# Performance work log

Measured on AMD Instinct MI355X. Metric: run time of the kernel, lower is better.

## Reference

```python
import jax, jax.numpy as jnp
import numpy as np

H = 256

def setup_inputs() -> dict:
    key = jax.random.key(0)
    ks = jax.random.split(key, 9)
    s = 1.0 / np.sqrt(H)
    x = jax.random.normal(ks[0], (8, 2048, H), dtype=jnp.float32)
    Wq = jax.random.uniform(ks[1], (H, H), jnp.float32, -s, s)
    bq = jax.random.uniform(ks[2], (H,), jnp.float32, -s, s)
    Wk = jax.random.uniform(ks[3], (H, H), jnp.float32, -s, s)
    bk = jax.random.uniform(ks[4], (H,), jnp.float32, -s, s)
    Wv = jax.random.uniform(ks[5], (H, H), jnp.float32, -s, s)
    bv = jax.random.uniform(ks[6], (H,), jnp.float32, -s, s)
    Ww = jax.random.uniform(ks[7], (H, 1), jnp.float32, -s, s)
    bw = jax.random.uniform(ks[8], (1,), jnp.float32, -s, s)
    return {"x": x, "Wq": Wq, "bq": bq, "Wk": Wk, "bk": bk,
            "Wv": Wv, "bv": bv, "Ww": Ww, "bw": bw}

def reference(x, Wq, bq, Wk, bk, Wv, bv, Ww, bw):
    # x: (B, N, H) — cross-asset attention over N assets
    q = x @ Wq + bq
    k = x @ Wk + bk
    v = x @ Wv + bv
    scale = 1.0 / jnp.sqrt(jnp.asarray(q.shape[-1], q.dtype))
    beta = jnp.einsum('bnd,bmd->bnm', q, k) * scale  # (B, N, N)
    beta = jax.nn.softmax(beta, axis=-1)
    # original: sum(value[:,None] * beta[...,None], dim=2) == beta @ v
    out = jnp.einsum('bnm,bmd->bnd', beta, v)
    final_scores = (out @ Ww + bw)[..., 0]  # (B, N)
    return final_scores
```

## Files before the change

### kernel.cpp

```cpp
#include <hip/hip_runtime.h>

#define H 256
#define NB 2048
#define BATCH 8
#define NSPLIT 4
#define KSPAN (NB / NSPLIT)

typedef unsigned short u16;
using bf16x8 = __attribute__((ext_vector_type(8))) __bf16;
using f32x4  = __attribute__((ext_vector_type(4))) float;

__device__ __forceinline__ u16 f2bf(float f) {
    union { float f; unsigned u; } v; v.f = f;
    unsigned r = v.u + 0x7fffu + ((v.u >> 16) & 1u);
    return (u16)(r >> 16);
}

__global__ __launch_bounds__(256) void weights_kernel(
        const float* __restrict__ Wq, const float* __restrict__ Wk,
        const float* __restrict__ Wv, const float* __restrict__ Ww,
        u16* __restrict__ wqt, u16* __restrict__ wkt, float* __restrict__ wvw) {
    int n = blockIdx.x, k = threadIdx.x;
    wqt[n * H + k] = f2bf(Wq[k * H + n]);
    wkt[n * H + k] = f2bf(Wk[k * H + n]);
    float p = Wv[n * H + k] * Ww[k];
    for (int o = 32; o; o >>= 1) p += __shfl_xor(p, o);
    __shared__ float red[4];
    int w = threadIdx.x >> 6, lane = threadIdx.x & 63;
    if (lane == 0) red[w] = p;
    __syncthreads();
    if (threadIdx.x == 0) wvw[n] = red[0] + red[1] + red[2] + red[3];
}

__global__ __launch_bounds__(256) void cvtu_kernel(
        const float* __restrict__ x, const float* __restrict__ wvw,
        const float* __restrict__ bv, const float* __restrict__ Ww,
        u16* __restrict__ xbf, float* __restrict__ uu) {
    int lane = threadIdx.x & 63;
    int row  = blockIdx.x * 4 + (threadIdx.x >> 6);
    float4 xv = *(const float4*)(x + row * H + lane * 4);
    ushort4 o;
    o.x = f2bf(xv.x); o.y = f2bf(xv.y); o.z = f2bf(xv.z); o.w = f2bf(xv.w);
    *(ushort4*)(xbf + row * H + lane * 4) = o;
    float4 wv = *(const float4*)(wvw + lane * 4);
    float s = xv.x * wv.x + xv.y * wv.y + xv.z * wv.z + xv.w * wv.w;
    float4 bvv = *(const float4*)(bv + lane * 4);
    float4 www = *(const float4*)(Ww + lane * 4);
    float c = bvv.x * www.x + bvv.y * www.y + bvv.z * www.z + bvv.w * www.w;
    for (int o2 = 32; o2; o2 >>= 1) { s += __shfl_xor(s, o2); c += __shfl_xor(c, o2); }
    if (lane == 0) uu[row] = s + c;
}

__global__ __launch_bounds__(256) void proj_kernel(
        const u16* __restrict__ xbf, const u16* __restrict__ wqt, const u16* __restrict__ wkt,
        const float* __restrict__ bq, const float* __restrict__ bk,
        u16* __restrict__ qbf, u16* __restrict__ kbf) {
    __shared__ u16 bt[64 * 264];
    const u16* wt      = blockIdx.z ? wkt : wqt;
    const float* bias  = blockIdx.z ? bk : bq;
    u16* outp          = blockIdx.z ? kbf : qbf;
    const float sc     = blockIdx.z ? 1.0f : 0.0625f;

    int tid = threadIdx.x;
    int mb = blockIdx.x * 64, nb = blockIdx.y * 64;

    for (int it = 0; it < 8; ++it) {
        int c = it * 256 + tid;
        int row = c >> 5, col = (c & 31) * 8;
        *(uint4*)&bt[row * 264 + col] = *(const uint4*)(wt + (nb + row) * H + col);
    }
    __syncthreads();

    int w = tid >> 6, lane = tid & 63;
    int l15 = lane & 15, quad = lane >> 4;

    bf16x8 a[8];
    const u16* abase = xbf + (mb + w * 16 + l15) * H + quad * 8;
    for (int ks = 0; ks < 8; ++ks) a[ks] = *(const bf16x8*)(abase + ks * 32);

    f32x4 acc[4] = {};
    for (int ks = 0; ks < 8; ++ks)
        for (int t = 0; t < 4; ++t) {
            bf16x8 b = *(const bf16x8*)&bt[(t * 16 + l15) * 264 + ks * 32 + quad * 8];
            acc[t] = __builtin_amdgcn_mfma_f32_16x16x32_bf16(a[ks], b, acc[t], 0, 0, 0);
        }

    int m = mb + w * 16 + quad * 4;
    for (int t = 0; t < 4; ++t) {
        int n = nb + t * 16 + l15;
        float bsn = bias[n];
        for (int r = 0; r < 4; ++r)
            outp[(m + r) * H + n] = f2bf((acc[t][r] + bsn) * sc);
    }
}

__global__ __launch_bounds__(256) void attn_kernel(
        const u16* __restrict__ qbf, const u16* __restrict__ kbf,
        const float* __restrict__ u,
        float* __restrict__ pnum, float* __restrict__ pden) {
    __shared__ u16 kt[64 * 264];
    __shared__ float ut[64];
    int tid = threadIdx.x;
    int b = blockIdx.y, qb = blockIdx.x * 64, sp = blockIdx.z;
    int w = tid >> 6, lane = tid & 63, l15 = lane & 15, quad = lane >> 4;

    bf16x8 aq[8];
    const u16* qbase = qbf + (size_t)(b * NB + qb + w * 16 + l15) * H + quad * 8;
    for (int ks = 0; ks < 8; ++ks) aq[ks] = *(const bf16x8*)(qbase + ks * 32);

    float ls[4] = {0.f, 0.f, 0.f, 0.f};
    float as[4] = {0.f, 0.f, 0.f, 0.f};

    const int kb0 = sp * KSPAN;
    for (int kb = kb0; kb < kb0 + KSPAN; kb += 64) {
        const u16* ksrc = kbf + (size_t)(b * NB + kb) * H;
        for (int it = 0; it < 8; ++it) {
            int c = it * 256 + tid;
            int row = c >> 5, col = (c & 31) * 8;
            *(uint4*)&kt[row * 264 + col] = *(const uint4*)(ksrc + row * H + col);
        }
        if (tid < 64) ut[tid] = u[b * NB + kb + tid];
        __syncthreads();

        f32x4 acc[4] = {};
        for (int ks = 0; ks < 8; ++ks)
            for (int t = 0; t < 4; ++t) {
                bf16x8 bfr = *(const bf16x8*)&kt[(t * 16 + l15) * 264 + ks * 32 + quad * 8];
                acc[t] = __builtin_amdgcn_mfma_f32_16x16x32_bf16(aq[ks], bfr, acc[t], 0, 0, 0);
            }

        float uv[4];
        for (int t = 0; t < 4; ++t) uv[t] = ut[t * 16 + l15];

        for (int r = 0; r < 4; ++r) {
            float p0 = __expf(acc[0][r]), p1 = __expf(acc[1][r]);
            float p2 = __expf(acc[2][r]), p3 = __expf(acc[3][r]);
            ls[r] += (p0 + p1) + (p2 + p3);
            as[r] += (p0 * uv[0] + p1 * uv[1]) + (p2 * uv[2] + p3 * uv[3]);
        }
        __syncthreads();
    }

    for (int r = 0; r < 4; ++r) {
        for (int o = 1; o < 16; o <<= 1) {
            ls[r] += __shfl_xor(ls[r], o);
            as[r] += __shfl_xor(as[r], o);
        }
    }
    if (l15 == 0) {
        size_t base = (size_t)(sp * BATCH + b) * NB + qb + w * 16 + quad * 4;
        for (int r = 0; r < 4; ++r) {
            pnum[base + r] = as[r];
            pden[base + r] = ls[r];
        }
    }
}

__global__ __launch_bounds__(256) void finalize_kernel(
        const float* __restrict__ pnum, const float* __restrict__ pden,
        const float* __restrict__ bw, float* __restrict__ out) {
    int i = blockIdx.x * 256 + threadIdx.x;
    float num = 0.f, den = 0.f;
    for (int sp = 0; sp < NSPLIT; ++sp) {
        num += pnum[sp * (BATCH * NB) + i];
        den += pden[sp * (BATCH * NB) + i];
    }
    out[i] = num / den + bw[0];
}

extern "C" void kernel_launch(void* const* d_in, const int* in_sizes, int n_in,
                              void* d_out, int out_size, void* d_ws, size_t ws_size,
                              hipStream_t stream) {
    (void)in_sizes; (void)n_in; (void)out_size; (void)ws_size;
    const float* x  = (const float*)d_in[0];
    const float* Wq = (const float*)d_in[1];
    const float* bq = (const float*)d_in[2];
    const float* Wk = (const float*)d_in[3];
    const float* bk = (const float*)d_in[4];
    const float* Wv = (const float*)d_in[5];
    const float* bv = (const float*)d_in[6];
    const float* Ww = (const float*)d_in[7];
    const float* bw = (const float*)d_in[8];
    float* out = (float*)d_out;

    u16* xbf = (u16*)d_ws;
    u16* qbf = xbf + 4194304;
    u16* kbf = qbf + 4194304;
    u16* wqt = kbf + 4194304;
    u16* wkt = wqt + 65536;
    float* wvw  = (float*)(wkt + 65536);
    float* uu   = wvw + 256;
    float* pnum = uu + 16384;
    float* pden = pnum + NSPLIT * BATCH * NB;

    hipLaunchKernelGGL(weights_kernel, dim3(256), dim3(256), 0, stream,
                       Wq, Wk, Wv, Ww, wqt, wkt, wvw);
    hipLaunchKernelGGL(cvtu_kernel, dim3(4096), dim3(256), 0, stream,
                       x, wvw, bv, Ww, xbf, uu);
    hipLaunchKernelGGL(proj_kernel, dim3(256, 4, 2), dim3(256), 0, stream,
                       xbf, wqt, wkt, bq, bk, qbf, kbf);
    hipLaunchKernelGGL(attn_kernel, dim3(32, 8, NSPLIT), dim3(256), 0, stream,
                       qbf, kbf, uu, pnum, pden);
    hipLaunchKernelGGL(finalize_kernel, dim3(64), dim3(256), 0, stream,
                       pnum, pden, bw, out);
}
```

Measured before the change: 129.4 us.

## Fold Wq·Wkᵀ into one bilinear matrix and attend against x directly

Precomputes A = Wq·Wkᵀ (scaled) so scores become (x·A)·xᵀ. Query-side bias terms cancel in the softmax, and the key bias term is folded into per-key weights exp(x·Wk·bq). This drops the separate K projection and its bf16 buffer, so keys are read straight from the bf16 x. It also doubles the query rows per block (128), and raises the key split from 4 to 8 to keep enough blocks in flight. The risks are extra rounding, since the composed A matrix and the exp weights are applied in bf16/fp32, and a serial per-thread dot product in prep_kernel.

```diff
diff --git a/kernel.cpp b/kernel.cpp
--- a/kernel.cpp
+++ b/kernel.cpp
@@ -3,7 +3,7 @@
 #define H 256
 #define NB 2048
 #define BATCH 8
-#define NSPLIT 4
+#define NSPLIT 8
 #define KSPAN (NB / NSPLIT)
 
 typedef unsigned short u16;
@@ -16,26 +16,38 @@
     return (u16)(r >> 16);
 }
 
-__global__ __launch_bounds__(256) void weights_kernel(
+__global__ __launch_bounds__(256) void prep_kernel(
         const float* __restrict__ Wq, const float* __restrict__ Wk,
         const float* __restrict__ Wv, const float* __restrict__ Ww,
-        u16* __restrict__ wqt, u16* __restrict__ wkt, float* __restrict__ wvw) {
-    int n = blockIdx.x, k = threadIdx.x;
-    wqt[n * H + k] = f2bf(Wq[k * H + n]);
-    wkt[n * H + k] = f2bf(Wk[k * H + n]);
-    float p = Wv[n * H + k] * Ww[k];
-    for (int o = 32; o; o >>= 1) p += __shfl_xor(p, o);
-    __shared__ float red[4];
-    int w = threadIdx.x >> 6, lane = threadIdx.x & 63;
-    if (lane == 0) red[w] = p;
+        const float* __restrict__ bq,
+        u16* __restrict__ aT, float* __restrict__ wvw, float* __restrict__ kbv) {
+    int f = blockIdx.x, t = threadIdx.x;
+    __shared__ float wkf[H];
+    __shared__ float redp[4], redr[4];
+    float wkval = Wk[f * H + t];
+    wkf[t] = wkval;
+    float p = Wv[f * H + t] * Ww[t];
+    float r = wkval * bq[t];
     __syncthreads();
-    if (threadIdx.x == 0) wvw[n] = red[0] + red[1] + red[2] + red[3];
+    float s = 0.f;
+    #pragma unroll 8
+    for (int d = 0; d < H; ++d) s += Wq[t * H + d] * wkf[d];
+    aT[f * H + t] = f2bf(s * 0.0625f);
+    for (int o = 32; o; o >>= 1) { p += __shfl_xor(p, o); r += __shfl_xor(r, o); }
+    int w = t >> 6, lane = t & 63;
+    if (lane == 0) { redp[w] = p; redr[w] = r; }
+    __syncthreads();
+    if (t == 0) {
+        wvw[f] = redp[0] + redp[1] + redp[2] + redp[3];
+        kbv[f] = redr[0] + redr[1] + redr[2] + redr[3];
+    }
 }
 
 __global__ __launch_bounds__(256) void cvtu_kernel(
         const float* __restrict__ x, const float* __restrict__ wvw,
-        const float* __restrict__ bv, const float* __restrict__ Ww,
-        u16* __restrict__ xbf, float* __restrict__ uu) {
+        const float* __restrict__ kbv, const float* __restrict__ bv,
+        const float* __restrict__ Ww,
+        u16* __restrict__ xbf, float* __restrict__ ue, float* __restrict__ ee) {
     int lane = threadIdx.x & 63;
     int row  = blockIdx.x * 4 + (threadIdx.x >> 6);
     float4 xv = *(const float4*)(x + row * H + lane * 4);
@@ -44,114 +56,127 @@
     *(ushort4*)(xbf + row * H + lane * 4) = o;
     float4 wv = *(const float4*)(wvw + lane * 4);
     float s = xv.x * wv.x + xv.y * wv.y + xv.z * wv.z + xv.w * wv.w;
+    float4 kv = *(const float4*)(kbv + lane * 4);
+    float d = xv.x * kv.x + xv.y * kv.y + xv.z * kv.z + xv.w * kv.w;
     float4 bvv = *(const float4*)(bv + lane * 4);
     float4 www = *(const float4*)(Ww + lane * 4);
     float c = bvv.x * www.x + bvv.y * www.y + bvv.z * www.z + bvv.w * www.w;
-    for (int o2 = 32; o2; o2 >>= 1) { s += __shfl_xor(s, o2); c += __shfl_xor(c, o2); }
-    if (lane == 0) uu[row] = s + c;
-}
-
-__global__ __launch_bounds__(256) void proj_kernel(
-        const u16* __restrict__ xbf, const u16* __restrict__ wqt, const u16* __restrict__ wkt,
-        const float* __restrict__ bq, const float* __restrict__ bk,
-        u16* __restrict__ qbf, u16* __restrict__ kbf) {
+    for (int o2 = 32; o2; o2 >>= 1) {
+        s += __shfl_xor(s, o2); d += __shfl_xor(d, o2); c += __shfl_xor(c, o2);
+    }
+    if (lane == 0) {
+        float e = __expf(d * 0.0625f);
+        ue[row] = e * (s + c);
+        ee[row] = e;
+    }
+}
+
+__global__ __launch_bounds__(256) void projT_kernel(
+        const u16* __restrict__ xbf, const u16* __restrict__ aT,
+        u16* __restrict__ T) {
     __shared__ u16 bt[64 * 264];
-    const u16* wt      = blockIdx.z ? wkt : wqt;
-    const float* bias  = blockIdx.z ? bk : bq;
-    u16* outp          = blockIdx.z ? kbf : qbf;
-    const float sc     = blockIdx.z ? 1.0f : 0.0625f;
-
     int tid = threadIdx.x;
-    int mb = blockIdx.x * 64, nb = blockIdx.y * 64;
+    int mb = blockIdx.x * 128, nb = blockIdx.y * 64;
 
     for (int it = 0; it < 8; ++it) {
         int c = it * 256 + tid;
         int row = c >> 5, col = (c & 31) * 8;
-        *(uint4*)&bt[row * 264 + col] = *(const uint4*)(wt + (nb + row) * H + col);
+        *(uint4*)&bt[row * 264 + col] = *(const uint4*)(aT + (nb + row) * H + col);
     }
     __syncthreads();
 
     int w = tid >> 6, lane = tid & 63;
     int l15 = lane & 15, quad = lane >> 4;
 
-    bf16x8 a[8];
-    const u16* abase = xbf + (mb + w * 16 + l15) * H + quad * 8;
-    for (int ks = 0; ks < 8; ++ks) a[ks] = *(const bf16x8*)(abase + ks * 32);
-
-    f32x4 acc[4] = {};
+    bf16x8 a[2][8];
+    for (int mi = 0; mi < 2; ++mi) {
+        const u16* abase = xbf + (mb + w * 32 + mi * 16 + l15) * H + quad * 8;
+        for (int ks = 0; ks < 8; ++ks) a[mi][ks] = *(const bf16x8*)(abase + ks * 32);
+    }
+
+    f32x4 acc[2][4] = {};
     for (int ks = 0; ks < 8; ++ks)
         for (int t = 0; t < 4; ++t) {
             bf16x8 b = *(const bf16x8*)&bt[(t * 16 + l15) * 264 + ks * 32 + quad * 8];
-            acc[t] = __builtin_amdgcn_mfma_f32_16x16x32_bf16(a[ks], b, acc[t], 0, 0, 0);
-        }
-
-    int m = mb + w * 16 + quad * 4;
-    for (int t = 0; t < 4; ++t) {
-        int n = nb + t * 16 + l15;
-        float bsn = bias[n];
-        for (int r = 0; r < 4; ++r)
-            outp[(m + r) * H + n] = f2bf((acc[t][r] + bsn) * sc);
+            acc[0][t] = __builtin_amdgcn_mfma_f32_16x16x32_bf16(a[0][ks], b, acc[0][t], 0, 0, 0);
+            acc[1][t] = __builtin_amdgcn_mfma_f32_16x16x32_bf16(a[1][ks], b, acc[1][t], 0, 0, 0);
+        }
+
+    for (int mi = 0; mi < 2; ++mi) {
+        int m = mb + w * 32 + mi * 16 + quad * 4;
+        for (int t = 0; t < 4; ++t) {
+            int n = nb + t * 16 + l15;
+            for (int r = 0; r < 4; ++r)
+                T[(m + r) * H + n] = f2bf(acc[mi][t][r]);
+        }
     }
 }
 
 __global__ __launch_bounds__(256) void attn_kernel(
-        const u16* __restrict__ qbf, const u16* __restrict__ kbf,
-        const float* __restrict__ u,
+        const u16* __restrict__ T, const u16* __restrict__ xbf,
+        const float* __restrict__ ue, const float* __restrict__ ee,
         float* __restrict__ pnum, float* __restrict__ pden) {
     __shared__ u16 kt[64 * 264];
-    __shared__ float ut[64];
+    __shared__ float utile[64], etile[64];
     int tid = threadIdx.x;
-    int b = blockIdx.y, qb = blockIdx.x * 64, sp = blockIdx.z;
+    int b = blockIdx.y, qb = blockIdx.x * 128, sp = blockIdx.z;
     int w = tid >> 6, lane = tid & 63, l15 = lane & 15, quad = lane >> 4;
 
-    bf16x8 aq[8];
-    const u16* qbase = qbf + (size_t)(b * NB + qb + w * 16 + l15) * H + quad * 8;
-    for (int ks = 0; ks < 8; ++ks) aq[ks] = *(const bf16x8*)(qbase + ks * 32);
-
-    float ls[4] = {0.f, 0.f, 0.f, 0.f};
-    float as[4] = {0.f, 0.f, 0.f, 0.f};
+    bf16x8 aq[2][8];
+    for (int mi = 0; mi < 2; ++mi) {
+        const u16* qbase = T + (size_t)(b * NB + qb + w * 32 + mi * 16 + l15) * H + quad * 8;
+        for (int ks = 0; ks < 8; ++ks) aq[mi][ks] = *(const bf16x8*)(qbase + ks * 32);
+    }
+
+    float ls[2][4] = {}, as_[2][4] = {};
 
     const int kb0 = sp * KSPAN;
     for (int kb = kb0; kb < kb0 + KSPAN; kb += 64) {
-        const u16* ksrc = kbf + (size_t)(b * NB + kb) * H;
+        const u16* ksrc = xbf + (size_t)(b * NB + kb) * H;
         for (int it = 0; it < 8; ++it) {
             int c = it * 256 + tid;
             int row = c >> 5, col = (c & 31) * 8;
             *(uint4*)&kt[row * 264 + col] = *(const uint4*)(ksrc + row * H + col);
         }
-        if (tid < 64) ut[tid] = u[b * NB + kb + tid];
+        if (tid < 64) utile[tid] = ue[b * NB + kb + tid];
+        else if (tid < 128) etile[tid - 64] = ee[b * NB + kb + (tid - 64)];
         __syncthreads();
 
-        f32x4 acc[4] = {};
+        f32x4 acc[2][4] = {};
         for (int ks = 0; ks < 8; ++ks)
             for (int t = 0; t < 4; ++t) {
                 bf16x8 bfr = *(const bf16x8*)&kt[(t * 16 + l15) * 264 + ks * 32 + quad * 8];
-                acc[t] = __builtin_amdgcn_mfma_f32_16x16x32_bf16(aq[ks], bfr, acc[t], 0, 0, 0);
-            }
-
-        float uv[4];
-        for (int t = 0; t < 4; ++t) uv[t] = ut[t * 16 + l15];
-
-        for (int r = 0; r < 4; ++r) {
-            float p0 = __expf(acc[0][r]), p1 = __expf(acc[1][r]);
-            float p2 = __expf(acc[2][r]), p3 = __expf(acc[3][r]);
-            ls[r] += (p0 + p1) + (p2 + p3);
-            as[r] += (p0 * uv[0] + p1 * uv[1]) + (p2 * uv[2] + p3 * uv[3]);
-        }
+                acc[0][t] = __builtin_amdgcn_mfma_f32_16x16x32_bf16(aq[0][ks], bfr, acc[0][t], 0, 0, 0);
+                acc[1][t] = __builtin_amdgcn_mfma_f32_16x16x32_bf16(aq[1][ks], bfr, acc[1][t], 0, 0, 0);
+            }
+
+        float uv[4], ev[4];
+        for (int t = 0; t < 4; ++t) { uv[t] = utile[t * 16 + l15]; ev[t] = etile[t * 16 + l15]; }
+
+        for (int mi = 0; mi < 2; ++mi)
+            for (int r = 0; r < 4; ++r) {
+                float p0 = __expf(acc[mi][0][r]), p1 = __expf(acc[mi][1][r]);
+                float p2 = __expf(acc[mi][2][r]), p3 = __expf(acc[mi][3][r]);
+                ls[mi][r]  += (p0 * ev[0] + p1 * ev[1]) + (p2 * ev[2] + p3 * ev[3]);
+                as_[mi][r] += (p0 * uv[0] + p1 * uv[1]) + (p2 * uv[2] + p3 * uv[3]);
+            }
         __syncthreads();
     }
 
-    for (int r = 0; r < 4; ++r) {
-        for (int o = 1; o < 16; o <<= 1) {
-            ls[r] += __shfl_xor(ls[r], o);
-            as[r] += __shfl_xor(as[r], o);
-        }
-    }
+    for (int mi = 0; mi < 2; ++mi)
+        for (int r = 0; r < 4; ++r)
+            for (int o = 1; o < 16; o <<= 1) {
+                ls[mi][r]  += __shfl_xor(ls[mi][r], o);
+                as_[mi][r] += __shfl_xor(as_[mi][r], o);
+            }
+
     if (l15 == 0) {
-        size_t base = (size_t)(sp * BATCH + b) * NB + qb + w * 16 + quad * 4;
-        for (int r = 0; r < 4; ++r) {
-            pnum[base + r] = as[r];
-            pden[base + r] = ls[r];
+        for (int mi = 0; mi < 2; ++mi) {
+            size_t base = (size_t)(sp * BATCH + b) * NB + qb + w * 32 + mi * 16 + quad * 4;
+            for (int r = 0; r < 4; ++r) {
+                pnum[base + r] = as_[mi][r];
+                pden[base + r] = ls[mi][r];
+            }
         }
     }
 }
@@ -176,7 +201,7 @@
     const float* Wq = (const float*)d_in[1];
     const float* bq = (const float*)d_in[2];
     const float* Wk = (const float*)d_in[3];
-    const float* bk = (const float*)d_in[4];
+    const float* bk = (const float*)d_in[4];  (void)bk;
     const float* Wv = (const float*)d_in[5];
     const float* bv = (const float*)d_in[6];
     const float* Ww = (const float*)d_in[7];
@@ -184,23 +209,23 @@
     float* out = (float*)d_out;
 
     u16* xbf = (u16*)d_ws;
-    u16* qbf = xbf + 4194304;
-    u16* kbf = qbf + 4194304;
-    u16* wqt = kbf + 4194304;
-    u16* wkt = wqt + 65536;
-    float* wvw  = (float*)(wkt + 65536);
-    float* uu   = wvw + 256;
-    float* pnum = uu + 16384;
+    u16* Tbf = xbf + 4194304;
+    u16* aT  = Tbf + 4194304;
+    float* wvw = (float*)(aT + 65536);
+    float* kbv = wvw + 256;
+    float* ue  = kbv + 256;
+    float* ee  = ue + 16384;
+    float* pnum = ee + 16384;
     float* pden = pnum + NSPLIT * BATCH * NB;
 
-    hipLaunchKernelGGL(weights_kernel, dim3(256), dim3(256), 0, stream,
-                       Wq, Wk, Wv, Ww, wqt, wkt, wvw);
+    hipLaunchKernelGGL(prep_kernel, dim3(256), dim3(256), 0, stream,
+                       Wq, Wk, Wv, Ww, bq, aT, wvw, kbv);
     hipLaunchKernelGGL(cvtu_kernel, dim3(4096), dim3(256), 0, stream,
-                       x, wvw, bv, Ww, xbf, uu);
-    hipLaunchKernelGGL(proj_kernel, dim3(256, 4, 2), dim3(256), 0, stream,
-                       xbf, wqt, wkt, bq, bk, qbf, kbf);
-    hipLaunchKernelGGL(attn_kernel, dim3(32, 8, NSPLIT), dim3(256), 0, stream,
-                       qbf, kbf, uu, pnum, pden);
+                       x, wvw, kbv, bv, Ww, xbf, ue, ee);
+    hipLaunchKernelGGL(projT_kernel, dim3(128, 4), dim3(256), 0, stream,
+                       xbf, aT, Tbf);
+    hipLaunchKernelGGL(attn_kernel, dim3(16, 8, NSPLIT), dim3(256), 0, stream,
+                       Tbf, xbf, ue, ee, pnum, pden);
     hipLaunchKernelGGL(finalize_kernel, dim3(64), dim3(256), 0, stream,
                        pnum, pden, bw, out);
 }
```

After: 158.9 us. 1.23x slower.
